# Kernel optimization log

Hardware: AMD Instinct MI355X
Metric: run time of the kernel (lower is better)

## Reference

```python
import jax, jax.numpy as jnp
import numpy as np

NU, NB, NI, D, L = 30000, 10000, 60000, 64, 2
E_UB, E_UI, E_BI = 400000, 800000, 800000


def _graphs(rng, na, nb, ne):
    # random bipartite graph [na, nb] with ne edges; returns Laplacian-normalized
    # symmetric propagation edge list (size 2*ne over na+nb nodes) and the
    # row-normalized aggregation edge values (original MultiCBR preprocessing).
    r = rng.integers(0, na, ne).astype(np.int32)
    c = rng.integers(0, nb, ne).astype(np.int32)
    da = np.bincount(r, minlength=na).astype(np.float32)  # row degrees
    db = np.bincount(c, minlength=nb).astype(np.float32)  # col degrees
    lap = 1.0 / ((np.sqrt(da[r]) + 1e-8) * (np.sqrt(db[c]) + 1e-8))
    prop_rows = np.concatenate([r, c + na]).astype(np.int32)
    prop_cols = np.concatenate([c + na, r]).astype(np.int32)
    prop_vals = np.concatenate([lap, lap]).astype(np.float32)
    agg_vals = (1.0 / (da[r] + 1e-8)).astype(np.float32)  # diag(1/rowsum) @ G
    return prop_rows, prop_cols, prop_vals, r, c, agg_vals


def setup_inputs() -> dict:
    rng = np.random.default_rng(0)
    key = jax.random.key(0)
    ku, kb, ki = jax.random.split(key, 3)
    ub = _graphs(rng, NU, NB, E_UB)
    ui = _graphs(rng, NU, NI, E_UI)
    bi = _graphs(rng, NB, NI, E_BI)
    xav = lambda n: float(np.sqrt(2.0 / (n + D)))  # xavier_normal std
    return {
        "users_feature": jax.random.normal(ku, (NU, D), jnp.float32) * xav(NU),
        "bundles_feature": jax.random.normal(kb, (NB, D), jnp.float32) * xav(NB),
        "items_feature": jax.random.normal(ki, (NI, D), jnp.float32) * xav(NI),
        "ub_rows": jnp.asarray(ub[0]), "ub_cols": jnp.asarray(ub[1]), "ub_vals": jnp.asarray(ub[2]),
        "ui_rows": jnp.asarray(ui[0]), "ui_cols": jnp.asarray(ui[1]), "ui_vals": jnp.asarray(ui[2]),
        "bi_rows": jnp.asarray(bi[0]), "bi_cols": jnp.asarray(bi[1]), "bi_vals": jnp.asarray(bi[2]),
        "bi_agg_rows": jnp.asarray(bi[3]), "bi_agg_cols": jnp.asarray(bi[4]), "bi_agg_vals": jnp.asarray(bi[5]),
        "ui_agg_rows": jnp.asarray(ui[3]), "ui_agg_cols": jnp.asarray(ui[4]), "ui_agg_vals": jnp.asarray(ui[5]),
        "ub_layer_coefs": jnp.full((L + 1,), 1.0 / (L + 1), jnp.float32),
        "ui_layer_coefs": jnp.full((L + 1,), 1.0 / (L + 1), jnp.float32),
        "bi_layer_coefs": jnp.full((L + 1,), 1.0 / (L + 1), jnp.float32),
        "modal_coefs": jnp.asarray([0.4, 0.3, 0.3], jnp.float32),
    }


def _spmm(rows, cols, vals, feat, n):
    # sparse [n, n_src] @ feat : gather + weighted segment-sum
    return jax.ops.segment_sum(vals[:, None] * feat[cols], rows, num_segments=n)


def _l2norm(x):
    # torch F.normalize(p=2, dim=1)
    return x / jnp.maximum(jnp.linalg.norm(x, axis=1, keepdims=True), 1e-12)


def _propagate(rows, cols, vals, a, b, coefs):
    feat = jnp.concatenate([a, b], axis=0)
    n = feat.shape[0]
    acc = coefs[0] * feat  # layer-0 (un-normalized, as in original)
    for i in range(L):
        feat = _spmm(rows, cols, vals, feat, n)
        acc = acc + coefs[i + 1] * _l2norm(feat)
    return acc[: a.shape[0]], acc[a.shape[0]:]


def reference(users_feature, bundles_feature, items_feature,
              ub_rows, ub_cols, ub_vals,
              ui_rows, ui_cols, ui_vals,
              bi_rows, bi_cols, bi_vals,
              bi_agg_rows, bi_agg_cols, bi_agg_vals,
              ui_agg_rows, ui_agg_cols, ui_agg_vals,
              ub_layer_coefs, ui_layer_coefs, bi_layer_coefs, modal_coefs):
    # test=True path of get_multi_modal_representations
    ub_u, ub_b = _propagate(ub_rows, ub_cols, ub_vals, users_feature, bundles_feature, ub_layer_coefs)
    ui_u, ui_i = _propagate(ui_rows, ui_cols, ui_vals, users_feature, items_feature, ui_layer_coefs)
    bi_b, bi_i = _propagate(bi_rows, bi_cols, bi_vals, bundles_feature, items_feature, bi_layer_coefs)
    ui_b = _spmm(bi_agg_rows, bi_agg_cols, bi_agg_vals, ui_i, NB)  # BI_agg @ UI_items
    bi_u = _spmm(ui_agg_rows, ui_agg_cols, ui_agg_vals, bi_i, NU)  # UI_agg @ BI_items
    users_rep = modal_coefs[0] * ub_u + modal_coefs[1] * ui_u + modal_coefs[2] * bi_u
    bundles_rep = modal_coefs[0] * ub_b + modal_coefs[1] * ui_b + modal_coefs[2] * bi_b
    return users_rep, bundles_rep
```

## Files before the change

kernel.cpp:

```cpp
#include <hip/hip_runtime.h>

#define D 64

__device__ __forceinline__ float blo(unsigned u) { return __uint_as_float(u << 16); }
__device__ __forceinline__ float bhi(unsigned u) { return __uint_as_float(u & 0xffff0000u); }
__device__ __forceinline__ unsigned rne(float f) {
    unsigned u = __float_as_uint(f);
    return (u + 0x7fffu + ((u >> 16) & 1u)) >> 16;
}
__device__ __forceinline__ unsigned packbf(float a, float b) {
    unsigned ub = __float_as_uint(b);
    return rne(a) | ((ub + 0x7fffu + ((ub >> 16) & 1u)) & 0xffff0000u);
}
__device__ __forceinline__ void add4(float4* p, float a, float b, float c, float d) {
    float4 o = *p; o.x += a; o.y += b; o.z += c; o.w += d; *p = o;
}

__global__ void to_bf16_kernel(const float* __restrict__ u, const float* __restrict__ b,
                               const float* __restrict__ it,
                               unsigned* __restrict__ SU, unsigned* __restrict__ SB,
                               unsigned* __restrict__ SI, int nU2, int nB2, int nI2) {
    int i = blockIdx.x * 256 + threadIdx.x;
    if (i < nU2) {
        float2 f = ((const float2*)u)[i];
        SU[i] = packbf(f.x, f.y);
    } else if (i < nU2 + nB2) {
        int j = i - nU2;
        float2 f = ((const float2*)b)[j];
        SB[j] = packbf(f.x, f.y);
    } else if (i < nU2 + nB2 + nI2) {
        int j = i - nU2 - nB2;
        float2 f = ((const float2*)it)[j];
        SI[j] = packbf(f.x, f.y);
    }
}

__global__ void hist_kernel(const int* __restrict__ r0, const int* __restrict__ r1,
                            const int* __restrict__ r2,
                            int ne0, int ne1, int ne2, int n0, int n1, int n2,
                            int* __restrict__ histG) {
    __shared__ int h[256];
    int t = threadIdx.x;
    int g = blockIdx.x >> 8, blk = blockIdx.x & 255;
    const int* rows = (g == 0) ? r0 : (g == 1) ? r1 : r2;
    int ne = (g == 0) ? ne0 : (g == 1) ? ne1 : ne2;
    unsigned n = (unsigned)((g == 0) ? n0 : (g == 1) ? n1 : n2);
    h[t] = 0;
    __syncthreads();
    int C = (ne + 255) >> 8;
    int e0 = blk * C, e1 = min(ne, e0 + C);
    for (int e = e0 + t; e < e1; e += 256) {
        unsigned b = ((unsigned)rows[e] << 8) / n;
        atomicAdd(&h[b], 1);
    }
    __syncthreads();
    histG[((((g << 8) | t)) << 8) | blk] = h[t];
}

__global__ void scan1_kernel(const int* __restrict__ deg, int* __restrict__ rs,
                             int* __restrict__ bsum, int n) {
    __shared__ int tmp[256];
    int t = threadIdx.x;
    int g = blockIdx.x * 256 + t;
    int v = (g < n) ? deg[g] : 0;
    tmp[t] = v;
    __syncthreads();
    for (int off = 1; off < 256; off <<= 1) {
        int x = (t >= off) ? tmp[t - off] : 0;
        __syncthreads();
        tmp[t] += x;
        __syncthreads();
    }
    if (g < n) rs[g] = tmp[t] - v;
    if (t == 255) bsum[blockIdx.x] = tmp[255];
}

__global__ void scan2_kernel(int* __restrict__ bsum, int B) {
    __shared__ int tmp[1024];
    int t = threadIdx.x;
    int v = (t < B) ? bsum[t] : 0;
    tmp[t] = v;
    __syncthreads();
    for (int off = 1; off < 1024; off <<= 1) {
        int x = (t >= off) ? tmp[t - off] : 0;
        __syncthreads();
        tmp[t] += x;
        __syncthreads();
    }
    if (t < B) bsum[t] = tmp[t] - v;
}

__global__ void scan3_kernel(int* __restrict__ rs, const int* __restrict__ bsum, int n) {
    int g = blockIdx.x * blockDim.x + threadIdx.x;
    if (g < n) rs[g] += bsum[g >> 8];
}

__global__ void bucket_scatter_kernel(const int* __restrict__ r0, const int* __restrict__ c0,
                                      const int* __restrict__ r1, const int* __restrict__ c1,
                                      const int* __restrict__ r2, const int* __restrict__ c2,
                                      int ne0, int ne1, int ne2, int n0, int n1, int n2,
                                      const int* __restrict__ hofs, unsigned* __restrict__ ebuf) {
    __shared__ int cur[256];
    int t = threadIdx.x;
    int g = blockIdx.x >> 8, blk = blockIdx.x & 255;
    const int* rows = (g == 0) ? r0 : (g == 1) ? r1 : r2;
    const int* cols = (g == 0) ? c0 : (g == 1) ? c1 : c2;
    int ne = (g == 0) ? ne0 : (g == 1) ? ne1 : ne2;
    int n  = (g == 0) ? n0  : (g == 1) ? n1  : n2;
    cur[t] = hofs[((((g << 8) | t)) << 8) | blk];
    __syncthreads();
    int C = (ne + 255) >> 8;
    int e0 = blk * C, e1 = min(ne, e0 + C);
    for (int e = e0 + t; e < e1; e += 256) {
        int r = rows[e];
        unsigned b = ((unsigned)r << 8) / (unsigned)n;
        int rb0 = ((int)b * n + 255) >> 8;
        int pos = atomicAdd(&cur[b], 1);
        ebuf[pos] = ((unsigned)(r - rb0) << 23) | (unsigned)cols[e];
    }
}

__global__ void sort_bucket_kernel(const unsigned* __restrict__ ebuf, const int* __restrict__ hofs,
                                   int* __restrict__ rs0, int* __restrict__ rs1, int* __restrict__ rs2,
                                   float* __restrict__ isd0, float* __restrict__ isd1,
                                   float* __restrict__ isd2, int* __restrict__ ccol,
                                   int ne0, int ne1, int ne2, int n0, int n1, int n2) {
    __shared__ int cnt[512];
    __shared__ int pfx[512];
    int t = threadIdx.x;
    int g = blockIdx.x >> 8, b = blockIdx.x & 255;
    int ne = (g == 0) ? ne0 : (g == 1) ? ne1 : ne2;
    int n  = (g == 0) ? n0  : (g == 1) ? n1  : n2;
    int O  = (g == 0) ? 0   : (g == 1) ? ne0 : ne0 + ne1;
    int*   rs  = (g == 0) ? rs0  : (g == 1) ? rs1  : rs2;
    float* isd = (g == 0) ? isd0 : (g == 1) ? isd1 : isd2;
    int rb0 = (b * n + 255) >> 8;
    int rb1 = ((b + 1) * n + 255) >> 8;
    int R = rb1 - rb0;
    cnt[t] = 0; cnt[t + 256] = 0;
    __syncthreads();
    int base = hofs[(((g << 8) | b)) << 8];
    int end  = (b == 255) ? (O + ne) : hofs[(((g << 8) | (b + 1))) << 8];
    for (int e = base + t; e < end; e += 256)
        atomicAdd(&cnt[ebuf[e] >> 23], 1);
    __syncthreads();
    pfx[t] = cnt[t]; pfx[t + 256] = cnt[t + 256];
    __syncthreads();
    for (int off = 1; off < 512; off <<= 1) {
        int v0 = (t >= off) ? pfx[t - off] : 0;
        int v1 = ((t + 256) >= off) ? pfx[t + 256 - off] : 0;
        __syncthreads();
        pfx[t] += v0; pfx[t + 256] += v1;
        __syncthreads();
    }
    int c0 = cnt[t],       e0 = pfx[t] - c0;
    int c1 = cnt[t + 256], e1 = pfx[t + 256] - c1;
    if (t < R) {
        rs[rb0 + t] = base + e0 - O;
        isd[rb0 + t] = 1.0f / (sqrtf((float)c0) + 1e-8f);
    }
    if (t + 256 < R) {
        rs[rb0 + t + 256] = base + e1 - O;
        isd[rb0 + t + 256] = 1.0f / (sqrtf((float)c1) + 1e-8f);
    }
    __syncthreads();
    cnt[t] = base + e0; cnt[t + 256] = base + e1;
    __syncthreads();
    for (int e = base + t; e < end; e += 256) {
        unsigned p = ebuf[e];
        int pos = atomicAdd(&cnt[p >> 23], 1);
        ccol[pos] = (int)(p & 0x7fffffu);
    }
    if (b == 255 && t == 0) rs[n] = ne;
}

struct GA {
    const int* rs; const int* ccol; const float* isd;
    const unsigned* srcA; const unsigned* srcB; int na;
    const float* inA; const float* inB;
    unsigned* feat_out; float* dst0; void* dst1;
    const float* coefs; const float* modalp; int mi; int n;
};

template <bool FIRST, bool ASSIGN1, bool BF16DST1>
__global__ void spmm_norm_kernel(GA A, GA B, int ntot) {
    int row = blockIdx.x * (blockDim.x >> 6) + (threadIdx.x >> 6);
    if (row >= ntot) return;
    GA G; int r;
    if (row < A.n) { G = A; r = row; }
    else           { G = B; r = row - A.n; if (r >= G.n) return; }
    int lane = threadIdx.x & 63;
    int g = lane >> 3, q = lane & 7;
    int s = G.rs[r], e = G.rs[r + 1];
    float isr = G.isd[r];
    const unsigned* src; int coff;
    if (FIRST && r < G.na) { src = G.srcB; coff = G.na; }
    else                   { src = G.srcA; coff = 0; }
    const float* isdp = G.isd;
    const int* cc = G.ccol;
    float acc[8];
#pragma unroll
    for (int j = 0; j < 8; ++j) acc[j] = 0.f;
    int k = s + g;
    for (; k + 8 < e; k += 16) {
        int c0 = cc[k];
        int c1 = cc[k + 8];
        float v0 = isr * isdp[c0];
        float v1 = isr * isdp[c1];
        uint4 f0 = *(const uint4*)(src + (size_t)(c0 - coff) * 32 + (q << 2));
        uint4 f1 = *(const uint4*)(src + (size_t)(c1 - coff) * 32 + (q << 2));
        acc[0] = fmaf(v0, blo(f0.x), acc[0]); acc[1] = fmaf(v0, bhi(f0.x), acc[1]);
        acc[2] = fmaf(v0, blo(f0.y), acc[2]); acc[3] = fmaf(v0, bhi(f0.y), acc[3]);
        acc[4] = fmaf(v0, blo(f0.z), acc[4]); acc[5] = fmaf(v0, bhi(f0.z), acc[5]);
        acc[6] = fmaf(v0, blo(f0.w), acc[6]); acc[7] = fmaf(v0, bhi(f0.w), acc[7]);
        acc[0] = fmaf(v1, blo(f1.x), acc[0]); acc[1] = fmaf(v1, bhi(f1.x), acc[1]);
        acc[2] = fmaf(v1, blo(f1.y), acc[2]); acc[3] = fmaf(v1, bhi(f1.y), acc[3]);
        acc[4] = fmaf(v1, blo(f1.z), acc[4]); acc[5] = fmaf(v1, bhi(f1.z), acc[5]);
        acc[6] = fmaf(v1, blo(f1.w), acc[6]); acc[7] = fmaf(v1, bhi(f1.w), acc[7]);
    }
    if (k < e) {
        int c0 = cc[k];
        float v0 = isr * isdp[c0];
        uint4 f0 = *(const uint4*)(src + (size_t)(c0 - coff) * 32 + (q << 2));
        acc[0] = fmaf(v0, blo(f0.x), acc[0]); acc[1] = fmaf(v0, bhi(f0.x), acc[1]);
        acc[2] = fmaf(v0, blo(f0.y), acc[2]); acc[3] = fmaf(v0, bhi(f0.y), acc[3]);
        acc[4] = fmaf(v0, blo(f0.z), acc[4]); acc[5] = fmaf(v0, bhi(f0.z), acc[5]);
        acc[6] = fmaf(v0, blo(f0.w), acc[6]); acc[7] = fmaf(v0, bhi(f0.w), acc[7]);
    }
#pragma unroll
    for (int o = 8; o < 64; o <<= 1) {
#pragma unroll
        for (int j = 0; j < 8; ++j) acc[j] += __shfl_xor(acc[j], o, 64);
    }
    float s2 = 0.f;
#pragma unroll
    for (int j = 0; j < 8; ++j) s2 += acc[j] * acc[j];
#pragma unroll
    for (int o = 1; o < 8; o <<= 1) s2 += __shfl_xor(s2, o, 64);
    if (g != 0) return;
    float inv = 1.0f / fmaxf(sqrtf(s2), 1e-12f);
    float mm = G.modalp[G.mi];
    size_t ro = (size_t)r * D + (q << 3);
    float ctb[8];
    if (FIRST) {
        uint4 fw;
        fw.x = packbf(acc[0], acc[1]); fw.y = packbf(acc[2], acc[3]);
        fw.z = packbf(acc[4], acc[5]); fw.w = packbf(acc[6], acc[7]);
        *(uint4*)(G.feat_out + (size_t)r * 32 + (q << 2)) = fw;
        const float* ib = (r < G.na) ? (G.inA + ro) : (G.inB + (size_t)(r - G.na) * D + (q << 3));
        float4 a0 = *(const float4*)ib;
        float4 a1 = *(const float4*)(ib + 4);
        float c0 = G.coefs[0], c1m = G.coefs[1] * inv;
        ctb[0] = mm * fmaf(c0, a0.x, c1m * acc[0]);
        ctb[1] = mm * fmaf(c0, a0.y, c1m * acc[1]);
        ctb[2] = mm * fmaf(c0, a0.z, c1m * acc[2]);
        ctb[3] = mm * fmaf(c0, a0.w, c1m * acc[3]);
        ctb[4] = mm * fmaf(c0, a1.x, c1m * acc[4]);
        ctb[5] = mm * fmaf(c0, a1.y, c1m * acc[5]);
        ctb[6] = mm * fmaf(c0, a1.z, c1m * acc[6]);
        ctb[7] = mm * fmaf(c0, a1.w, c1m * acc[7]);
    } else {
        float mc = mm * G.coefs[2] * inv;
#pragma unroll
        for (int j = 0; j < 8; ++j) ctb[j] = mc * acc[j];
    }
    if (r < G.na) {
        add4((float4*)(G.dst0 + ro), ctb[0], ctb[1], ctb[2], ctb[3]);
        add4((float4*)(G.dst0 + ro + 4), ctb[4], ctb[5], ctb[6], ctb[7]);
    } else if (BF16DST1) {
        unsigned* p = (unsigned*)G.dst1 + (size_t)(r - G.na) * 32 + (q << 2);
        if (!(FIRST && ASSIGN1)) {
            uint4 cur = *(const uint4*)p;
            ctb[0] += blo(cur.x); ctb[1] += bhi(cur.x);
            ctb[2] += blo(cur.y); ctb[3] += bhi(cur.y);
            ctb[4] += blo(cur.z); ctb[5] += bhi(cur.z);
            ctb[6] += blo(cur.w); ctb[7] += bhi(cur.w);
        }
        uint4 w;
        w.x = packbf(ctb[0], ctb[1]); w.y = packbf(ctb[2], ctb[3]);
        w.z = packbf(ctb[4], ctb[5]); w.w = packbf(ctb[6], ctb[7]);
        *(uint4*)p = w;
    } else {
        float* d1 = (float*)G.dst1 + (size_t)(r - G.na) * D + (q << 3);
        add4((float4*)d1, ctb[0], ctb[1], ctb[2], ctb[3]);
        add4((float4*)(d1 + 4), ctb[4], ctb[5], ctb[6], ctb[7]);
    }
}

__global__ void agg2_kernel(const int* __restrict__ rsA, const int* __restrict__ ccA,
                            const unsigned* __restrict__ sA, float* __restrict__ oA,
                            int naA, int nA,
                            const int* __restrict__ rsB, const int* __restrict__ ccB,
                            const unsigned* __restrict__ sB, float* __restrict__ oB,
                            int naB, int nB) {
    int row = blockIdx.x * (blockDim.x >> 6) + (threadIdx.x >> 6);
    if (row >= nA + nB) return;
    const int* rs; const int* cc; const unsigned* src; float* out; int na; int r;
    if (row < nA) { rs = rsA; cc = ccA; src = sA; out = oA; na = naA; r = row; }
    else          { rs = rsB; cc = ccB; src = sB; out = oB; na = naB; r = row - nA; }
    int lane = threadIdx.x & 63;
    int g = lane >> 3, q = lane & 7;
    int s = rs[r], e = rs[r + 1];
    float acc[8];
#pragma unroll
    for (int j = 0; j < 8; ++j) acc[j] = 0.f;
    int k = s + g;
    for (; k + 8 < e; k += 16) {
        int c0 = cc[k] - na, c1 = cc[k + 8] - na;
        uint4 f0 = *(const uint4*)(src + (size_t)c0 * 32 + (q << 2));
        uint4 f1 = *(const uint4*)(src + (size_t)c1 * 32 + (q << 2));
        acc[0] += blo(f0.x) + blo(f1.x); acc[1] += bhi(f0.x) + bhi(f1.x);
        acc[2] += blo(f0.y) + blo(f1.y); acc[3] += bhi(f0.y) + bhi(f1.y);
        acc[4] += blo(f0.z) + blo(f1.z); acc[5] += bhi(f0.z) + bhi(f1.z);
        acc[6] += blo(f0.w) + blo(f1.w); acc[7] += bhi(f0.w) + bhi(f1.w);
    }
    if (k < e) {
        int c0 = cc[k] - na;
        uint4 f0 = *(const uint4*)(src + (size_t)c0 * 32 + (q << 2));
        acc[0] += blo(f0.x); acc[1] += bhi(f0.x);
        acc[2] += blo(f0.y); acc[3] += bhi(f0.y);
        acc[4] += blo(f0.z); acc[5] += bhi(f0.z);
        acc[6] += blo(f0.w); acc[7] += bhi(f0.w);
    }
#pragma unroll
    for (int o = 8; o < 64; o <<= 1) {
#pragma unroll
        for (int j = 0; j < 8; ++j) acc[j] += __shfl_xor(acc[j], o, 64);
    }
    if (g != 0) return;
    float ad = 1.0f / ((float)(e - s) + 1e-8f);
    float* p = out + (size_t)r * D + (q << 3);
    add4((float4*)p, ad * acc[0], ad * acc[1], ad * acc[2], ad * acc[3]);
    add4((float4*)(p + 4), ad * acc[4], ad * acc[5], ad * acc[6], ad * acc[7]);
}

extern "C" void kernel_launch(void* const* d_in, const int* in_sizes, int n_in,
                              void* d_out, int out_size, void* d_ws, size_t ws_size,
                              hipStream_t stream) {
    const float* users   = (const float*)d_in[0];
    const float* bundles = (const float*)d_in[1];
    const float* items   = (const float*)d_in[2];
    const int*   ub_rows = (const int*)d_in[3];
    const int*   ub_cols = (const int*)d_in[4];
    const int*   ui_rows = (const int*)d_in[6];
    const int*   ui_cols = (const int*)d_in[7];
    const int*   bi_rows = (const int*)d_in[9];
    const int*   bi_cols = (const int*)d_in[10];
    const float* ub_coefs = (const float*)d_in[18];
    const float* ui_coefs = (const float*)d_in[19];
    const float* bi_coefs = (const float*)d_in[20];
    const float* modal    = (const float*)d_in[21];

    const int NU_ = in_sizes[0] / D;
    const int NB_ = in_sizes[1] / D;
    const int NI_ = in_sizes[2] / D;
    const int ne_ub = in_sizes[3];
    const int ne_ui = in_sizes[6];
    const int ne_bi = in_sizes[9];

    const int n_ui = NU_ + NI_;
    const int n_bi = NB_ + NI_;
    const int n_ub = NU_ + NB_;

    float* out = (float*)d_out;

    int*      rs_ui  = (int*)d_ws;
    int*      rs_bi  = rs_ui + 90112;
    int*      rs_ub  = rs_bi + 70144;
    float*    isd_ui = (float*)(rs_ub + 40192);
    float*    isd_bi = isd_ui + 90112;
    float*    isd_ub = isd_bi + 70144;
    int*      histG  = (int*)(isd_ub + 40192);
    int*      hofs   = histG + 196608;
    int*      bsum   = hofs + 196672;
    int*      ccol   = bsum + 1024;
    unsigned* SU     = (unsigned*)(ccol + 4000000);
    unsigned* SB     = SU + 960000;
    unsigned* SI     = SB + 320000;
    unsigned* ovl    = SI + 1920000;
    unsigned* ebuf   = ovl;
    unsigned* sfB_ui = ovl;
    unsigned* sfB_bi = sfB_ui + 2880000;
    unsigned* IT1b   = sfB_bi + 2240000;
    unsigned* IT2b   = IT1b + 1920000;
    unsigned* sfB_ub = IT1b;

    int* ccol_ui = ccol;
    int* ccol_bi = ccol + ne_ui;
    int* ccol_ub = ccol + ne_ui + ne_bi;

    float* out_u = out;
    float* out_b = out + (size_t)NU_ * D;

    hipMemsetAsync(out, 0, (size_t)n_ub * D * sizeof(float), stream);
    {
        int tot2 = (NU_ + NB_ + NI_) * 32;
        to_bf16_kernel<<<(tot2 + 255) / 256, 256, 0, stream>>>(
            users, bundles, items, SU, SB, SI, NU_ * 32, NB_ * 32, NI_ * 32);
    }

    hist_kernel<<<768, 256, 0, stream>>>(ui_rows, bi_rows, ub_rows,
                                         ne_ui, ne_bi, ne_ub, n_ui, n_bi, n_ub, histG);
    scan1_kernel<<<768, 256, 0, stream>>>(histG, hofs, bsum, 196608);
    scan2_kernel<<<1, 1024, 0, stream>>>(bsum, 768);
    scan3_kernel<<<768, 256, 0, stream>>>(hofs, bsum, 196608);
    bucket_scatter_kernel<<<768, 256, 0, stream>>>(
        ui_rows, ui_cols, bi_rows, bi_cols, ub_rows, ub_cols,
        ne_ui, ne_bi, ne_ub, n_ui, n_bi, n_ub, hofs, ebuf);
    sort_bucket_kernel<<<768, 256, 0, stream>>>(
        ebuf, hofs, rs_ui, rs_bi, rs_ub, isd_ui, isd_bi, isd_ub, ccol,
        ne_ui, ne_bi, ne_ub, n_ui, n_bi, n_ub);

    GA gUI = { rs_ui, ccol_ui, isd_ui, SU, SI, NU_, users, items,
               sfB_ui, out_u, (void*)IT1b, ui_coefs, modal, 1, n_ui };
    GA gBI = { rs_bi, ccol_bi, isd_bi, SB, SI, NB_, bundles, items,
               sfB_bi, out_b, (void*)IT2b, bi_coefs, modal, 2, n_bi };
    GA gUB = { rs_ub, ccol_ub, isd_ub, SU, SB, NU_, users, bundles,
               sfB_ub, out_u, (void*)out_b, ub_coefs, modal, 0, n_ub };
    GA gUI2 = gUI; gUI2.srcA = sfB_ui;
    GA gBI2 = gBI; gBI2.srcA = sfB_bi;
    GA gUB2 = gUB; gUB2.srcA = sfB_ub;

    int ntotL = n_ui + n_bi;
    spmm_norm_kernel<true,  true,  true ><<<(ntotL + 3) / 4, 256, 0, stream>>>(gUI,  gBI,  ntotL);
    spmm_norm_kernel<false, false, true ><<<(ntotL + 3) / 4, 256, 0, stream>>>(gUI2, gBI2, ntotL);

    agg2_kernel<<<(NU_ + NB_ + 3) / 4, 256, 0, stream>>>(
        rs_ui, ccol_ui, IT2b, out_u, NU_, NU_,
        rs_bi, ccol_bi, IT1b, out_b, NB_, NB_);

    spmm_norm_kernel<true,  false, false><<<(n_ub + 3) / 4, 256, 0, stream>>>(gUB,  gUB,  n_ub);
    spmm_norm_kernel<false, false, false><<<(n_ub + 3) / 4, 256, 0, stream>>>(gUB2, gUB2, n_ub);
}
```

Before: 524.9 us.

## Pre-scale layer-2 features, drop output memset, use packed f2 math, finer buckets

The layer-1 output is pre-multiplied by isr^2, so the second SpMM pass becomes a plain sum without per-edge isd lookups. The first pass writes its output directly instead of accumulating, which removes the output memset. Accumulation uses packed float2 vector math. The bucket sort moves to 512 buckets per graph with smaller per-bucket sort blocks, and histG is aliased onto ccol to save workspace. The risk is correctness: the UI/BI pass must write every user and bundle row before the later accumulating passes read them.

```diff
diff --git a/kernel.cpp b/kernel.cpp
--- a/kernel.cpp
+++ b/kernel.cpp
@@ -1,9 +1,14 @@
 #include <hip/hip_runtime.h>
 
 #define D 64
+
+typedef float f2 __attribute__((ext_vector_type(2)));
 
 __device__ __forceinline__ float blo(unsigned u) { return __uint_as_float(u << 16); }
 __device__ __forceinline__ float bhi(unsigned u) { return __uint_as_float(u & 0xffff0000u); }
+__device__ __forceinline__ f2 up2(unsigned u) {
+    f2 r; r.x = blo(u); r.y = bhi(u); return r;
+}
 __device__ __forceinline__ unsigned rne(float f) {
     unsigned u = __float_as_uint(f);
     return (u + 0x7fffu + ((u >> 16) & 1u)) >> 16;
@@ -35,26 +40,28 @@
     }
 }
 
+
 __global__ void hist_kernel(const int* __restrict__ r0, const int* __restrict__ r1,
                             const int* __restrict__ r2,
                             int ne0, int ne1, int ne2, int n0, int n1, int n2,
                             int* __restrict__ histG) {
-    __shared__ int h[256];
+    __shared__ int h[512];
     int t = threadIdx.x;
     int g = blockIdx.x >> 8, blk = blockIdx.x & 255;
     const int* rows = (g == 0) ? r0 : (g == 1) ? r1 : r2;
     int ne = (g == 0) ? ne0 : (g == 1) ? ne1 : ne2;
     unsigned n = (unsigned)((g == 0) ? n0 : (g == 1) ? n1 : n2);
-    h[t] = 0;
+    h[t] = 0; h[t + 256] = 0;
     __syncthreads();
     int C = (ne + 255) >> 8;
     int e0 = blk * C, e1 = min(ne, e0 + C);
     for (int e = e0 + t; e < e1; e += 256) {
-        unsigned b = ((unsigned)rows[e] << 8) / n;
+        unsigned b = ((unsigned)rows[e] << 9) / n;
         atomicAdd(&h[b], 1);
     }
     __syncthreads();
-    histG[((((g << 8) | t)) << 8) | blk] = h[t];
+    histG[(((g << 9) | t) << 8) | blk] = h[t];
+    histG[(((g << 9) | (t + 256)) << 8) | blk] = h[t + 256];
 }
 
 __global__ void scan1_kernel(const int* __restrict__ deg, int* __restrict__ rs,
@@ -76,18 +83,21 @@
 }
 
 __global__ void scan2_kernel(int* __restrict__ bsum, int B) {
-    __shared__ int tmp[1024];
+    __shared__ int tmp[2048];
     int t = threadIdx.x;
-    int v = (t < B) ? bsum[t] : 0;
-    tmp[t] = v;
-    __syncthreads();
-    for (int off = 1; off < 1024; off <<= 1) {
-        int x = (t >= off) ? tmp[t - off] : 0;
-        __syncthreads();
-        tmp[t] += x;
-        __syncthreads();
-    }
-    if (t < B) bsum[t] = tmp[t] - v;
+    int v0 = (t < B) ? bsum[t] : 0;
+    int v1 = (t + 1024 < B) ? bsum[t + 1024] : 0;
+    tmp[t] = v0; tmp[t + 1024] = v1;
+    __syncthreads();
+    for (int off = 1; off < 2048; off <<= 1) {
+        int a0 = (t >= off) ? tmp[t - off] : 0;
+        int a1 = ((t + 1024) >= off) ? tmp[t + 1024 - off] : 0;
+        __syncthreads();
+        tmp[t] += a0; tmp[t + 1024] += a1;
+        __syncthreads();
+    }
+    if (t < B) bsum[t] = tmp[t] - v0;
+    if (t + 1024 < B) bsum[t + 1024] = tmp[t + 1024] - v1;
 }
 
 __global__ void scan3_kernel(int* __restrict__ rs, const int* __restrict__ bsum, int n) {
@@ -100,21 +110,22 @@
                                       const int* __restrict__ r2, const int* __restrict__ c2,
                                       int ne0, int ne1, int ne2, int n0, int n1, int n2,
                                       const int* __restrict__ hofs, unsigned* __restrict__ ebuf) {
-    __shared__ int cur[256];
+    __shared__ int cur[512];
     int t = threadIdx.x;
     int g = blockIdx.x >> 8, blk = blockIdx.x & 255;
     const int* rows = (g == 0) ? r0 : (g == 1) ? r1 : r2;
     const int* cols = (g == 0) ? c0 : (g == 1) ? c1 : c2;
     int ne = (g == 0) ? ne0 : (g == 1) ? ne1 : ne2;
     int n  = (g == 0) ? n0  : (g == 1) ? n1  : n2;
-    cur[t] = hofs[((((g << 8) | t)) << 8) | blk];
+    cur[t] = hofs[(((g << 9) | t) << 8) | blk];
+    cur[t + 256] = hofs[(((g << 9) | (t + 256)) << 8) | blk];
     __syncthreads();
     int C = (ne + 255) >> 8;
     int e0 = blk * C, e1 = min(ne, e0 + C);
     for (int e = e0 + t; e < e1; e += 256) {
         int r = rows[e];
-        unsigned b = ((unsigned)r << 8) / (unsigned)n;
-        int rb0 = ((int)b * n + 255) >> 8;
+        unsigned b = ((unsigned)r << 9) / (unsigned)n;
+        int rb0 = ((int)b * n + 511) >> 9;
         int pos = atomicAdd(&cur[b], 1);
         ebuf[pos] = ((unsigned)(r - rb0) << 23) | (unsigned)cols[e];
     }
@@ -125,53 +136,47 @@
                                    float* __restrict__ isd0, float* __restrict__ isd1,
                                    float* __restrict__ isd2, int* __restrict__ ccol,
                                    int ne0, int ne1, int ne2, int n0, int n1, int n2) {
-    __shared__ int cnt[512];
-    __shared__ int pfx[512];
+    __shared__ int cnt[256];
+    __shared__ int pfx[256];
     int t = threadIdx.x;
-    int g = blockIdx.x >> 8, b = blockIdx.x & 255;
+    int g = blockIdx.x >> 9, b = blockIdx.x & 511;
     int ne = (g == 0) ? ne0 : (g == 1) ? ne1 : ne2;
     int n  = (g == 0) ? n0  : (g == 1) ? n1  : n2;
     int O  = (g == 0) ? 0   : (g == 1) ? ne0 : ne0 + ne1;
     int*   rs  = (g == 0) ? rs0  : (g == 1) ? rs1  : rs2;
     float* isd = (g == 0) ? isd0 : (g == 1) ? isd1 : isd2;
-    int rb0 = (b * n + 255) >> 8;
-    int rb1 = ((b + 1) * n + 255) >> 8;
+    int rb0 = (b * n + 511) >> 9;
+    int rb1 = ((b + 1) * n + 511) >> 9;
     int R = rb1 - rb0;
-    cnt[t] = 0; cnt[t + 256] = 0;
-    __syncthreads();
-    int base = hofs[(((g << 8) | b)) << 8];
-    int end  = (b == 255) ? (O + ne) : hofs[(((g << 8) | (b + 1))) << 8];
+    cnt[t] = 0;
+    __syncthreads();
+    int base = hofs[((g << 9) | b) << 8];
+    int end  = (b == 511) ? (O + ne) : hofs[((g << 9) | (b + 1)) << 8];
     for (int e = base + t; e < end; e += 256)
         atomicAdd(&cnt[ebuf[e] >> 23], 1);
     __syncthreads();
-    pfx[t] = cnt[t]; pfx[t + 256] = cnt[t + 256];
-    __syncthreads();
-    for (int off = 1; off < 512; off <<= 1) {
-        int v0 = (t >= off) ? pfx[t - off] : 0;
-        int v1 = ((t + 256) >= off) ? pfx[t + 256 - off] : 0;
-        __syncthreads();
-        pfx[t] += v0; pfx[t + 256] += v1;
-        __syncthreads();
-    }
-    int c0 = cnt[t],       e0 = pfx[t] - c0;
-    int c1 = cnt[t + 256], e1 = pfx[t + 256] - c1;
+    pfx[t] = cnt[t];
+    __syncthreads();
+    for (int off = 1; off < 256; off <<= 1) {
+        int v = (t >= off) ? pfx[t - off] : 0;
+        __syncthreads();
+        pfx[t] += v;
+        __syncthreads();
+    }
+    int c0 = cnt[t], ex = pfx[t] - c0;
     if (t < R) {
-        rs[rb0 + t] = base + e0 - O;
+        rs[rb0 + t] = base + ex - O;
         isd[rb0 + t] = 1.0f / (sqrtf((float)c0) + 1e-8f);
     }
-    if (t + 256 < R) {
-        rs[rb0 + t + 256] = base + e1 - O;
-        isd[rb0 + t + 256] = 1.0f / (sqrtf((float)c1) + 1e-8f);
-    }
-    __syncthreads();
-    cnt[t] = base + e0; cnt[t + 256] = base + e1;
+    __syncthreads();
+    cnt[t] = base + ex;
     __syncthreads();
     for (int e = base + t; e < end; e += 256) {
         unsigned p = ebuf[e];
         int pos = atomicAdd(&cnt[p >> 23], 1);
         ccol[pos] = (int)(p & 0x7fffffu);
     }
-    if (b == 255 && t == 0) rs[n] = ne;
+    if (b == 511 && t == 0) rs[n] = ne;
 }
 
 struct GA {
@@ -182,7 +187,7 @@
     const float* coefs; const float* modalp; int mi; int n;
 };
 
-template <bool FIRST, bool ASSIGN1, bool BF16DST1>
+template <bool FIRST, bool A0, bool A1, bool BF16D1>
 __global__ void spmm_norm_kernel(GA A, GA B, int ntot) {
     int row = blockIdx.x * (blockDim.x >> 6) + (threadIdx.x >> 6);
     if (row >= ntot) return;
@@ -196,45 +201,66 @@
     const unsigned* src; int coff;
     if (FIRST && r < G.na) { src = G.srcB; coff = G.na; }
     else                   { src = G.srcA; coff = 0; }
+    src += (q << 2);
+    const int* cc = G.ccol;
     const float* isdp = G.isd;
-    const int* cc = G.ccol;
-    float acc[8];
-#pragma unroll
-    for (int j = 0; j < 8; ++j) acc[j] = 0.f;
+    f2 acc2[4];
+#pragma unroll
+    for (int j = 0; j < 4; ++j) acc2[j] = (f2){0.f, 0.f};
     int k = s + g;
-    for (; k + 8 < e; k += 16) {
-        int c0 = cc[k];
-        int c1 = cc[k + 8];
-        float v0 = isr * isdp[c0];
-        float v1 = isr * isdp[c1];
-        uint4 f0 = *(const uint4*)(src + (size_t)(c0 - coff) * 32 + (q << 2));
-        uint4 f1 = *(const uint4*)(src + (size_t)(c1 - coff) * 32 + (q << 2));
-        acc[0] = fmaf(v0, blo(f0.x), acc[0]); acc[1] = fmaf(v0, bhi(f0.x), acc[1]);
-        acc[2] = fmaf(v0, blo(f0.y), acc[2]); acc[3] = fmaf(v0, bhi(f0.y), acc[3]);
-        acc[4] = fmaf(v0, blo(f0.z), acc[4]); acc[5] = fmaf(v0, bhi(f0.z), acc[5]);
-        acc[6] = fmaf(v0, blo(f0.w), acc[6]); acc[7] = fmaf(v0, bhi(f0.w), acc[7]);
-        acc[0] = fmaf(v1, blo(f1.x), acc[0]); acc[1] = fmaf(v1, bhi(f1.x), acc[1]);
-        acc[2] = fmaf(v1, blo(f1.y), acc[2]); acc[3] = fmaf(v1, bhi(f1.y), acc[3]);
-        acc[4] = fmaf(v1, blo(f1.z), acc[4]); acc[5] = fmaf(v1, bhi(f1.z), acc[5]);
-        acc[6] = fmaf(v1, blo(f1.w), acc[6]); acc[7] = fmaf(v1, bhi(f1.w), acc[7]);
-    }
-    if (k < e) {
-        int c0 = cc[k];
-        float v0 = isr * isdp[c0];
-        uint4 f0 = *(const uint4*)(src + (size_t)(c0 - coff) * 32 + (q << 2));
-        acc[0] = fmaf(v0, blo(f0.x), acc[0]); acc[1] = fmaf(v0, bhi(f0.x), acc[1]);
-        acc[2] = fmaf(v0, blo(f0.y), acc[2]); acc[3] = fmaf(v0, bhi(f0.y), acc[3]);
-        acc[4] = fmaf(v0, blo(f0.z), acc[4]); acc[5] = fmaf(v0, bhi(f0.z), acc[5]);
-        acc[6] = fmaf(v0, blo(f0.w), acc[6]); acc[7] = fmaf(v0, bhi(f0.w), acc[7]);
-    }
+    if (FIRST) {
+        for (; k + 8 < e; k += 16) {
+            int c0 = cc[k], c1 = cc[k + 8];
+            float v0 = isdp[c0], v1 = isdp[c1];
+            uint4 f0 = *(const uint4*)(src + (size_t)(c0 - coff) * 32);
+            uint4 f1 = *(const uint4*)(src + (size_t)(c1 - coff) * 32);
+            f2 v02 = {v0, v0}, v12 = {v1, v1};
+            acc2[0] = v02 * up2(f0.x) + acc2[0];
+            acc2[1] = v02 * up2(f0.y) + acc2[1];
+            acc2[2] = v02 * up2(f0.z) + acc2[2];
+            acc2[3] = v02 * up2(f0.w) + acc2[3];
+            acc2[0] = v12 * up2(f1.x) + acc2[0];
+            acc2[1] = v12 * up2(f1.y) + acc2[1];
+            acc2[2] = v12 * up2(f1.z) + acc2[2];
+            acc2[3] = v12 * up2(f1.w) + acc2[3];
+        }
+        if (k < e) {
+            int c0 = cc[k];
+            float v0 = isdp[c0];
+            uint4 f0 = *(const uint4*)(src + (size_t)(c0 - coff) * 32);
+            f2 v02 = {v0, v0};
+            acc2[0] = v02 * up2(f0.x) + acc2[0];
+            acc2[1] = v02 * up2(f0.y) + acc2[1];
+            acc2[2] = v02 * up2(f0.z) + acc2[2];
+            acc2[3] = v02 * up2(f0.w) + acc2[3];
+        }
+    } else {
+        for (; k + 8 < e; k += 16) {
+            int c0 = cc[k], c1 = cc[k + 8];
+            uint4 f0 = *(const uint4*)(src + (size_t)c0 * 32);
+            uint4 f1 = *(const uint4*)(src + (size_t)c1 * 32);
+            acc2[0] += up2(f0.x); acc2[1] += up2(f0.y);
+            acc2[2] += up2(f0.z); acc2[3] += up2(f0.w);
+            acc2[0] += up2(f1.x); acc2[1] += up2(f1.y);
+            acc2[2] += up2(f1.z); acc2[3] += up2(f1.w);
+        }
+        if (k < e) {
+            int c0 = cc[k];
+            uint4 f0 = *(const uint4*)(src + (size_t)c0 * 32);
+            acc2[0] += up2(f0.x); acc2[1] += up2(f0.y);
+            acc2[2] += up2(f0.z); acc2[3] += up2(f0.w);
+        }
+    }
+    float a[8] = {acc2[0].x, acc2[0].y, acc2[1].x, acc2[1].y,
+                  acc2[2].x, acc2[2].y, acc2[3].x, acc2[3].y};
 #pragma unroll
     for (int o = 8; o < 64; o <<= 1) {
 #pragma unroll
-        for (int j = 0; j < 8; ++j) acc[j] += __shfl_xor(acc[j], o, 64);
+        for (int j = 0; j < 8; ++j) a[j] += __shfl_xor(a[j], o, 64);
     }
     float s2 = 0.f;
 #pragma unroll
-    for (int j = 0; j < 8; ++j) s2 += acc[j] * acc[j];
+    for (int j = 0; j < 8; ++j) s2 += a[j] * a[j];
 #pragma unroll
     for (int o = 1; o < 8; o <<= 1) s2 += __shfl_xor(s2, o, 64);
     if (g != 0) return;
@@ -243,33 +269,41 @@
     size_t ro = (size_t)r * D + (q << 3);
     float ctb[8];
     if (FIRST) {
+        float isr2 = isr * isr;
         uint4 fw;
-        fw.x = packbf(acc[0], acc[1]); fw.y = packbf(acc[2], acc[3]);
-        fw.z = packbf(acc[4], acc[5]); fw.w = packbf(acc[6], acc[7]);
+        fw.x = packbf(isr2 * a[0], isr2 * a[1]);
+        fw.y = packbf(isr2 * a[2], isr2 * a[3]);
+        fw.z = packbf(isr2 * a[4], isr2 * a[5]);
+        fw.w = packbf(isr2 * a[6], isr2 * a[7]);
         *(uint4*)(G.feat_out + (size_t)r * 32 + (q << 2)) = fw;
         const float* ib = (r < G.na) ? (G.inA + ro) : (G.inB + (size_t)(r - G.na) * D + (q << 3));
         float4 a0 = *(const float4*)ib;
         float4 a1 = *(const float4*)(ib + 4);
         float c0 = G.coefs[0], c1m = G.coefs[1] * inv;
-        ctb[0] = mm * fmaf(c0, a0.x, c1m * acc[0]);
-        ctb[1] = mm * fmaf(c0, a0.y, c1m * acc[1]);
-        ctb[2] = mm * fmaf(c0, a0.z, c1m * acc[2]);
-        ctb[3] = mm * fmaf(c0, a0.w, c1m * acc[3]);
-        ctb[4] = mm * fmaf(c0, a1.x, c1m * acc[4]);
-        ctb[5] = mm * fmaf(c0, a1.y, c1m * acc[5]);
-        ctb[6] = mm * fmaf(c0, a1.z, c1m * acc[6]);
-        ctb[7] = mm * fmaf(c0, a1.w, c1m * acc[7]);
+        ctb[0] = mm * fmaf(c0, a0.x, c1m * a[0]);
+        ctb[1] = mm * fmaf(c0, a0.y, c1m * a[1]);
+        ctb[2] = mm * fmaf(c0, a0.z, c1m * a[2]);
+        ctb[3] = mm * fmaf(c0, a0.w, c1m * a[3]);
+        ctb[4] = mm * fmaf(c0, a1.x, c1m * a[4]);
+        ctb[5] = mm * fmaf(c0, a1.y, c1m * a[5]);
+        ctb[6] = mm * fmaf(c0, a1.z, c1m * a[6]);
+        ctb[7] = mm * fmaf(c0, a1.w, c1m * a[7]);
     } else {
         float mc = mm * G.coefs[2] * inv;
 #pragma unroll
-        for (int j = 0; j < 8; ++j) ctb[j] = mc * acc[j];
+        for (int j = 0; j < 8; ++j) ctb[j] = mc * a[j];
     }
     if (r < G.na) {
-        add4((float4*)(G.dst0 + ro), ctb[0], ctb[1], ctb[2], ctb[3]);
-        add4((float4*)(G.dst0 + ro + 4), ctb[4], ctb[5], ctb[6], ctb[7]);
-    } else if (BF16DST1) {
+        if (A0) {
+            *(float4*)(G.dst0 + ro) = make_float4(ctb[0], ctb[1], ctb[2], ctb[3]);
+            *(float4*)(G.dst0 + ro + 4) = make_float4(ctb[4], ctb[5], ctb[6], ctb[7]);
+        } else {
+            add4((float4*)(G.dst0 + ro), ctb[0], ctb[1], ctb[2], ctb[3]);
+            add4((float4*)(G.dst0 + ro + 4), ctb[4], ctb[5], ctb[6], ctb[7]);
+        }
+    } else if (BF16D1) {
         unsigned* p = (unsigned*)G.dst1 + (size_t)(r - G.na) * 32 + (q << 2);
-        if (!(FIRST && ASSIGN1)) {
+        if (!A1) {
             uint4 cur = *(const uint4*)p;
             ctb[0] += blo(cur.x); ctb[1] += bhi(cur.x);
             ctb[2] += blo(cur.y); ctb[3] += bhi(cur.y);
@@ -300,38 +334,39 @@
     else          { rs = rsB; cc = ccB; src = sB; out = oB; na = naB; r = row - nA; }
     int lane = threadIdx.x & 63;
     int g = lane >> 3, q = lane & 7;
+    src += (q << 2);
     int s = rs[r], e = rs[r + 1];
-    float acc[8];
-#pragma unroll
-    for (int j = 0; j < 8; ++j) acc[j] = 0.f;
+    f2 acc2[4];
+#pragma unroll
+    for (int j = 0; j < 4; ++j) acc2[j] = (f2){0.f, 0.f};
     int k = s + g;
     for (; k + 8 < e; k += 16) {
         int c0 = cc[k] - na, c1 = cc[k + 8] - na;
-        uint4 f0 = *(const uint4*)(src + (size_t)c0 * 32 + (q << 2));
-        uint4 f1 = *(const uint4*)(src + (size_t)c1 * 32 + (q << 2));
-        acc[0] += blo(f0.x) + blo(f1.x); acc[1] += bhi(f0.x) + bhi(f1.x);
-        acc[2] += blo(f0.y) + blo(f1.y); acc[3] += bhi(f0.y) + bhi(f1.y);
-        acc[4] += blo(f0.z) + blo(f1.z); acc[5] += bhi(f0.z) + bhi(f1.z);
-        acc[6] += blo(f0.w) + blo(f1.w); acc[7] += bhi(f0.w) + bhi(f1.w);
+        uint4 f0 = *(const uint4*)(src + (size_t)c0 * 32);
+        uint4 f1 = *(const uint4*)(src + (size_t)c1 * 32);
+        acc2[0] += up2(f0.x); acc2[1] += up2(f0.y);
+        acc2[2] += up2(f0.z); acc2[3] += up2(f0.w);
+        acc2[0] += up2(f1.x); acc2[1] += up2(f1.y);
+        acc2[2] += up2(f1.z); acc2[3] += up2(f1.w);
     }
     if (k < e) {
         int c0 = cc[k] - na;
-        uint4 f0 = *(const uint4*)(src + (size_t)c0 * 32 + (q << 2));
-        acc[0] += blo(f0.x); acc[1] += bhi(f0.x);
-        acc[2] += blo(f0.y); acc[3] += bhi(f0.y);
-        acc[4] += blo(f0.z); acc[5] += bhi(f0.z);
-        acc[6] += blo(f0.w); acc[7] += bhi(f0.w);
-    }
+        uint4 f0 = *(const uint4*)(src + (size_t)c0 * 32);
+        acc2[0] += up2(f0.x); acc2[1] += up2(f0.y);
+        acc2[2] += up2(f0.z); acc2[3] += up2(f0.w);
+    }
+    float a[8] = {acc2[0].x, acc2[0].y, acc2[1].x, acc2[1].y,
+                  acc2[2].x, acc2[2].y, acc2[3].x, acc2[3].y};
 #pragma unroll
     for (int o = 8; o < 64; o <<= 1) {
 #pragma unroll
-        for (int j = 0; j < 8; ++j) acc[j] += __shfl_xor(acc[j], o, 64);
+        for (int j = 0; j < 8; ++j) a[j] += __shfl_xor(a[j], o, 64);
     }
     if (g != 0) return;
     float ad = 1.0f / ((float)(e - s) + 1e-8f);
     float* p = out + (size_t)r * D + (q << 3);
-    add4((float4*)p, ad * acc[0], ad * acc[1], ad * acc[2], ad * acc[3]);
-    add4((float4*)(p + 4), ad * acc[4], ad * acc[5], ad * acc[6], ad * acc[7]);
+    add4((float4*)p, ad * a[0], ad * a[1], ad * a[2], ad * a[3]);
+    add4((float4*)(p + 4), ad * a[4], ad * a[5], ad * a[6], ad * a[7]);
 }
 
 extern "C" void kernel_launch(void* const* d_in, const int* in_sizes, int n_in,
@@ -370,10 +405,10 @@
     float*    isd_ui = (float*)(rs_ub + 40192);
     float*    isd_bi = isd_ui + 90112;
     float*    isd_ub = isd_bi + 70144;
-    int*      histG  = (int*)(isd_ub + 40192);
-    int*      hofs   = histG + 196608;
-    int*      bsum   = hofs + 196672;
-    int*      ccol   = bsum + 1024;
+    int*      hofs   = (int*)(isd_ub + 40192);
+    int*      bsum   = hofs + 393280;
+    int*      ccol   = bsum + 2048;
+    int*      histG  = ccol;
     unsigned* SU     = (unsigned*)(ccol + 4000000);
     unsigned* SB     = SU + 960000;
     unsigned* SI     = SB + 320000;
@@ -392,7 +427,6 @@
     float* out_u = out;
     float* out_b = out + (size_t)NU_ * D;
 
-    hipMemsetAsync(out, 0, (size_t)n_ub * D * sizeof(float), stream);
     {
         int tot2 = (NU_ + NB_ + NI_) * 32;
         to_bf16_kernel<<<(tot2 + 255) / 256, 256, 0, stream>>>(
@@ -401,13 +435,13 @@
 
     hist_kernel<<<768, 256, 0, stream>>>(ui_rows, bi_rows, ub_rows,
                                          ne_ui, ne_bi, ne_ub, n_ui, n_bi, n_ub, histG);
-    scan1_kernel<<<768, 256, 0, stream>>>(histG, hofs, bsum, 196608);
-    scan2_kernel<<<1, 1024, 0, stream>>>(bsum, 768);
-    scan3_kernel<<<768, 256, 0, stream>>>(hofs, bsum, 196608);
+    scan1_kernel<<<1536, 256, 0, stream>>>(histG, hofs, bsum, 393216);
+    scan2_kernel<<<1, 1024, 0, stream>>>(bsum, 1536);
+    scan3_kernel<<<1536, 256, 0, stream>>>(hofs, bsum, 393216);
     bucket_scatter_kernel<<<768, 256, 0, stream>>>(
         ui_rows, ui_cols, bi_rows, bi_cols, ub_rows, ub_cols,
         ne_ui, ne_bi, ne_ub, n_ui, n_bi, n_ub, hofs, ebuf);
-    sort_bucket_kernel<<<768, 256, 0, stream>>>(
+    sort_bucket_kernel<<<1536, 256, 0, stream>>>(
         ebuf, hofs, rs_ui, rs_bi, rs_ub, isd_ui, isd_bi, isd_ub, ccol,
         ne_ui, ne_bi, ne_ub, n_ui, n_bi, n_ub);
 
@@ -422,13 +456,13 @@
     GA gUB2 = gUB; gUB2.srcA = sfB_ub;
 
     int ntotL = n_ui + n_bi;
-    spmm_norm_kernel<true,  true,  true ><<<(ntotL + 3) / 4, 256, 0, stream>>>(gUI,  gBI,  ntotL);
-    spmm_norm_kernel<false, false, true ><<<(ntotL + 3) / 4, 256, 0, stream>>>(gUI2, gBI2, ntotL);
+    spmm_norm_kernel<true,  true,  true,  true ><<<(ntotL + 3) / 4, 256, 0, stream>>>(gUI,  gBI,  ntotL);
+    spmm_norm_kernel<false, false, false, true ><<<(ntotL + 3) / 4, 256, 0, stream>>>(gUI2, gBI2, ntotL);
 
     agg2_kernel<<<(NU_ + NB_ + 3) / 4, 256, 0, stream>>>(
         rs_ui, ccol_ui, IT2b, out_u, NU_, NU_,
         rs_bi, ccol_bi, IT1b, out_b, NB_, NB_);
 
-    spmm_norm_kernel<true,  false, false><<<(n_ub + 3) / 4, 256, 0, stream>>>(gUB,  gUB,  n_ub);
-    spmm_norm_kernel<false, false, false><<<(n_ub + 3) / 4, 256, 0, stream>>>(gUB2, gUB2, n_ub);
-}
+    spmm_norm_kernel<true,  false, false, false><<<(n_ub + 3) / 4, 256, 0, stream>>>(gUB,  gUB,  n_ub);
+    spmm_norm_kernel<false, false, false, false><<<(n_ub + 3) / 4, 256, 0, stream>>>(gUB2, gUB2, n_ub);
+}
```

Measured after the change: 509.0 us. 1.03x faster.
